# Optimization experiments

Measured on AMD Instinct MI355X. Metric: run time of the kernel, lower is better.

The kernel has to match this reference:

```python
import jax, jax.numpy as jnp
import numpy as np


def dwconv3x3(x, w, b):
    # depthwise 3x3, stride 1, padding 1 (SAME); x: [B,C,H,W], w: [C,1,3,3], b: [C]
    y = jax.lax.conv_general_dilated(
        x, w, window_strides=(1, 1), padding='SAME',
        dimension_numbers=('NCHW', 'OIHW', 'NCHW'),
        feature_group_count=x.shape[1])
    return y + b[None, :, None, None]


def setup_inputs() -> dict:
    B, C, K, H, W = 16, 512, 128, 64, 64
    key = jax.random.key(0)
    ks = jax.random.split(key, 8)
    return {
        'x_q': jax.random.normal(ks[0], (B, C, H, W), jnp.float32),
        'x_kv': jax.random.normal(ks[1], (B, K, H, W), jnp.float32),
        'wq': jax.random.normal(ks[2], (C, 1, 3, 3), jnp.float32) * 0.1,
        'bq': jax.random.normal(ks[3], (C,), jnp.float32) * 0.1,
        'wk': jax.random.normal(ks[4], (K, 1, 3, 3), jnp.float32) * 0.1,
        'bk': jax.random.normal(ks[5], (K,), jnp.float32) * 0.1,
        'wv': jax.random.normal(ks[6], (K, 1, 3, 3), jnp.float32) * 0.1,
        'bv': jax.random.normal(ks[7], (K,), jnp.float32) * 0.1,
    }


def reference(x_q, x_kv, wq, bq, wk, bk, wv, bv):
    q = dwconv3x3(x_q, wq, bq)          # [B,C,H,W]
    k = dwconv3x3(x_kv, wk, bk)         # [B,K,H,W]
    v = dwconv3x3(x_kv, wv, bv)         # [B,K,H,W]
    B, C, H, W = q.shape
    Kp = k.shape[1]
    qf = q.reshape(B, C, H * W)         # [B,C,N]
    kf = k.reshape(B, Kp, H * W)        # [B,K,N]
    vf = v.reshape(B, Kp, H * W)        # [B,K,N]
    # attn_weights: [B,C,K], scaled by sqrt(num_prompt)
    aw = jnp.einsum('bcn,bkn->bck', qf, kf) / (Kp ** 0.5)
    aw = jax.nn.softmax(aw, axis=-1)
    n_keep = int(0.1 * C)               # static
    aw_t = jnp.swapaxes(aw, 1, 2)       # [B,K,C]
    _, idx = jax.lax.top_k(aw_t, n_keep)  # idx: [B,K,n_keep]
    bi = jnp.arange(B)[:, None, None]
    ki = jnp.arange(Kp)[None, :, None]
    mask_t = jnp.zeros_like(aw_t).at[bi, ki, idx].set(1.0)
    aw = aw * jnp.swapaxes(mask_t, 1, 2)  # [B,C,K]
    attn_out = jnp.einsum('bck,bkn->bcn', aw, vf).reshape(B, C, H, W)
    return (x_q + attn_out, aw)
```

## Files before the change

### kernel.cpp

```cpp
#include <hip/hip_runtime.h>

#define B_ 16
#define C_ 512
#define K_ 128
#define N_ 4096
#define NKEEP 51
#define NSPLIT 16

__global__ __launch_bounds__(256) void conv_kv_kernel(const float* __restrict__ xkv,
                               const float* __restrict__ wk, const float* __restrict__ bk,
                               const float* __restrict__ wv, const float* __restrict__ bv,
                               float* __restrict__ kb, float* __restrict__ vb) {
    int idx = blockIdx.x * 256 + threadIdx.x;
    int xs = (idx & 3) << 4;
    int y  = (idx >> 2) & 63;
    int k  = (idx >> 8) & 127;
    int b  = idx >> 15;
    const float* wkp = wk + k * 9;
    const float* wvp = wv + k * 9;
    const float* xp  = xkv + (size_t)(b * K_ + k) * N_;
    float ak[16], av[16];
    float bk0 = bk[k], bv0 = bv[k];
#pragma unroll
    for (int i = 0; i < 16; ++i) { ak[i] = bk0; av[i] = bv0; }
#pragma unroll
    for (int dy = 0; dy < 3; ++dy) {
        int yy = y + dy - 1;
        if (yy < 0 || yy > 63) continue;
        const float* row = xp + yy * 64 + xs;
        const float4* r4 = (const float4*)row;
        float4 m0 = r4[0], m1 = r4[1], m2 = r4[2], m3 = r4[3];
        float xrow[18];
        xrow[0] = (xs == 0) ? 0.f : row[-1];
        xrow[1] = m0.x;  xrow[2] = m0.y;  xrow[3] = m0.z;  xrow[4] = m0.w;
        xrow[5] = m1.x;  xrow[6] = m1.y;  xrow[7] = m1.z;  xrow[8] = m1.w;
        xrow[9] = m2.x;  xrow[10] = m2.y; xrow[11] = m2.z; xrow[12] = m2.w;
        xrow[13] = m3.x; xrow[14] = m3.y; xrow[15] = m3.z; xrow[16] = m3.w;
        xrow[17] = (xs == 48) ? 0.f : row[16];
        float ka = wkp[dy * 3], kb_ = wkp[dy * 3 + 1], kc_ = wkp[dy * 3 + 2];
        float va = wvp[dy * 3], vb_ = wvp[dy * 3 + 1], vc_ = wvp[dy * 3 + 2];
#pragma unroll
        for (int i = 0; i < 16; ++i) {
            ak[i] += xrow[i] * ka + xrow[i + 1] * kb_ + xrow[i + 2] * kc_;
            av[i] += xrow[i] * va + xrow[i + 1] * vb_ + xrow[i + 2] * vc_;
        }
    }
    size_t o = (size_t)(b * K_ + k) * N_ + y * 64 + xs;
    float4* kd = (float4*)(kb + o);
    float4* vd = (float4*)(vb + o);
#pragma unroll
    for (int m = 0; m < 4; ++m) {
        kd[m] = make_float4(ak[4*m], ak[4*m+1], ak[4*m+2], ak[4*m+3]);
        vd[m] = make_float4(av[4*m], av[4*m+1], av[4*m+2], av[4*m+3]);
    }
}

__global__ __launch_bounds__(256) void qk5_kernel(const float* __restrict__ xq,
                                                  const float* __restrict__ wq,
                                                  const float* __restrict__ bq,
                                                  const float* __restrict__ kb,
                                                  float* __restrict__ part) {
    __shared__ float qs[64][64];
    __shared__ float ks[64][128];
    int blk = blockIdx.x;
    int ct  = blk & 7;
    int ns  = (blk >> 3) & 15;
    int b   = blk >> 7;
    int c0  = ct * 64;
    int r0  = ns * 4;
    int tid = threadIdx.x;

    int c_l = tid >> 2;
    int xs  = (tid & 3) << 4;
    int k_l = tid >> 1;
    int nh  = (tid & 1) << 5;
    int cg4 = (tid & 15) * 4;
    int kg8 = (tid >> 4) * 8;

    const float* wp = wq + (size_t)(c0 + c_l) * 9;
    float w00=wp[0],w01=wp[1],w02=wp[2],w10=wp[3],w11=wp[4],w12=wp[5],w20=wp[6],w21=wp[7],w22=wp[8];
    float bias = bq[c0 + c_l];
    const float* xqp = xq + ((size_t)(b * C_) + c0 + c_l) * N_;
    const float* kbp = kb + ((size_t)(b * K_) + k_l) * N_;

    float acc[4][8];
#pragma unroll
    for (int i = 0; i < 4; ++i)
#pragma unroll
        for (int j = 0; j < 8; ++j) acc[i][j] = 0.f;

    for (int rr = 0; rr < 4; ++rr) {
        int r = r0 + rr;
        __syncthreads();
        {
            const float4* src = (const float4*)(kbp + r * 64 + nh);
#pragma unroll
            for (int m = 0; m < 8; ++m) {
                float4 v = src[m];
                int nn = nh + m * 4;
                ks[nn][k_l] = v.x; ks[nn + 1][k_l] = v.y;
                ks[nn + 2][k_l] = v.z; ks[nn + 3][k_l] = v.w;
            }
        }
        {
            float a16[16];
#pragma unroll
            for (int i = 0; i < 16; ++i) a16[i] = bias;
#pragma unroll
            for (int dy = 0; dy < 3; ++dy) {
                int yy = r + dy - 1;
                if (yy < 0 || yy > 63) continue;
                const float* row = xqp + yy * 64;
                float wa = (dy == 0) ? w00 : (dy == 1) ? w10 : w20;
                float wb = (dy == 0) ? w01 : (dy == 1) ? w11 : w21;
                float wc = (dy == 0) ? w02 : (dy == 1) ? w12 : w22;
                float p = (xs == 0) ? 0.f : row[xs - 1];
                float c = row[xs];
#pragma unroll
                for (int i = 0; i < 16; ++i) {
                    int x = xs + i;
                    float n = (x == 63) ? 0.f : row[x + 1];
                    a16[i] += p * wa + c * wb + n * wc;
                    p = c; c = n;
                }
            }
#pragma unroll
            for (int i = 0; i < 16; ++i) qs[xs + i][c_l] = a16[i];
        }
        __syncthreads();
#pragma unroll 4
        for (int nn = 0; nn < 64; ++nn) {
            float4 q4  = *(const float4*)&qs[nn][cg4];
            float4 k4a = *(const float4*)&ks[nn][kg8];
            float4 k4b = *(const float4*)&ks[nn][kg8 + 4];
            float qa[4] = {q4.x, q4.y, q4.z, q4.w};
            float kk[8] = {k4a.x, k4a.y, k4a.z, k4a.w, k4b.x, k4b.y, k4b.z, k4b.w};
#pragma unroll
            for (int i = 0; i < 4; ++i)
#pragma unroll
                for (int j = 0; j < 8; ++j) acc[i][j] += qa[i] * kk[j];
        }
    }
    float* dst = part + (((size_t)ns * B_ + b) * C_ + c0 + cg4) * K_ + kg8;
#pragma unroll
    for (int i = 0; i < 4; ++i) {
        *(float4*)(dst + (size_t)i * K_)     = make_float4(acc[i][0], acc[i][1], acc[i][2], acc[i][3]);
        *(float4*)(dst + (size_t)i * K_ + 4) = make_float4(acc[i][4], acc[i][5], acc[i][6], acc[i][7]);
    }
}

__global__ void softmax_kernel(const float* __restrict__ part, float* __restrict__ aw) {
    int tid  = threadIdx.x;
    int wave = tid >> 6;
    int lane = tid & 63;
    int row  = blockIdx.x * 4 + wave;
    float v0 = 0.f, v1 = 0.f;
#pragma unroll
    for (int ns = 0; ns < NSPLIT; ++ns) {
        const float* p = part + ((size_t)ns * B_ * C_ + row) * K_;
        v0 += p[lane];
        v1 += p[lane + 64];
    }
    const float scale = 0.08838834764831845f;
    v0 *= scale; v1 *= scale;
    float m = fmaxf(v0, v1);
#pragma unroll
    for (int s = 32; s >= 1; s >>= 1) m = fmaxf(m, __shfl_xor(m, s, 64));
    float e0 = __expf(v0 - m), e1 = __expf(v1 - m);
    float s = e0 + e1;
#pragma unroll
    for (int t = 32; t >= 1; t >>= 1) s += __shfl_xor(s, t, 64);
    float inv = 1.0f / s;
    float* q = aw + (size_t)row * K_;
    q[lane] = e0 * inv;
    q[lane + 64] = e1 * inv;
}

__global__ void topk_mask_kernel(float* __restrict__ aw) {
    int tid  = threadIdx.x;
    int wave = tid >> 6, lane = tid & 63;
    int col  = blockIdx.x * 4 + wave;
    int b = col >> 7, k = col & 127;
    float* base = aw + (size_t)(b * C_) * K_ + k;
    unsigned u[8];
#pragma unroll
    for (int j = 0; j < 8; ++j)
        u[j] = __float_as_uint(base[(size_t)(j * 64 + lane) * K_]);
    unsigned T = 0;
#pragma unroll
    for (int bit = 31; bit >= 0; --bit) {
        unsigned cand = T | (1u << bit);
        int cnt = 0;
#pragma unroll
        for (int j = 0; j < 8; ++j) cnt += (u[j] >= cand) ? 1 : 0;
#pragma unroll
        for (int s = 32; s >= 1; s >>= 1) cnt += __shfl_xor(cnt, s, 64);
        if (cnt >= NKEEP) T = cand;
    }
#pragma unroll
    for (int j = 0; j < 8; ++j)
        if (u[j] < T) base[(size_t)(j * 64 + lane) * K_] = 0.0f;
}

__global__ __launch_bounds__(256) void av_kernel(const float* __restrict__ aw,
                                                 const float* __restrict__ vb,
                                                 const float* __restrict__ xq,
                                                 float* __restrict__ out) {
    __shared__ float vs[16][260];
    __shared__ float aws[16][36];
    int blk  = blockIdx.x;
    int b    = blk >> 8;
    int rest = blk & 255;
    int c0 = (rest >> 4) * 32;
    int n0 = (rest & 15) * 256;
    int tid = threadIdx.x;
    int cg = tid >> 5;
    int ng = tid & 31;
    int k_l = tid >> 4;
    int nn0 = (tid & 15) * 16;

    float acc[4][8];
#pragma unroll
    for (int i = 0; i < 4; ++i)
#pragma unroll
        for (int j = 0; j < 8; ++j) acc[i][j] = 0.f;

    for (int kc = 0; kc < K_; kc += 16) {
        __syncthreads();
        {
            const float4* src = (const float4*)(vb + (size_t)(b * K_ + kc + k_l) * N_ + n0 + nn0);
            float4* dst = (float4*)&vs[k_l][nn0];
#pragma unroll
            for (int m = 0; m < 4; ++m) dst[m] = src[m];
        }
        {
            int i0 = tid * 2;
#pragma unroll
            for (int t2 = 0; t2 < 2; ++t2) {
                int i = i0 + t2;
                int cc = i >> 4;
                int kk = i & 15;
                aws[kk][cc] = aw[(size_t)(b * C_ + c0 + cc) * K_ + kc + kk];
            }
        }
        __syncthreads();
#pragma unroll
        for (int kk = 0; kk < 16; ++kk) {
            float4 a4  = *(const float4*)&aws[kk][cg * 4];
            float4 v4a = *(const float4*)&vs[kk][ng * 8];
            float4 v4b = *(const float4*)&vs[kk][ng * 8 + 4];
            float aa[4] = {a4.x, a4.y, a4.z, a4.w};
            float av[8] = {v4a.x, v4a.y, v4a.z, v4a.w, v4b.x, v4b.y, v4b.z, v4b.w};
#pragma unroll
            for (int i = 0; i < 4; ++i)
#pragma unroll
                for (int j = 0; j < 8; ++j) acc[i][j] += aa[i] * av[j];
        }
    }
#pragma unroll
    for (int i = 0; i < 4; ++i) {
        int c = c0 + cg * 4 + i;
        size_t base = (size_t)(b * C_ + c) * N_ + n0 + ng * 8;
        const float4* xp4 = (const float4*)(xq + base);
        float4* op4 = (float4*)(out + base);
        float4 x0 = xp4[0], x1 = xp4[1];
        float4 o0, o1;
        o0.x = x0.x + acc[i][0]; o0.y = x0.y + acc[i][1];
        o0.z = x0.z + acc[i][2]; o0.w = x0.w + acc[i][3];
        o1.x = x1.x + acc[i][4]; o1.y = x1.y + acc[i][5];
        o1.z = x1.z + acc[i][6]; o1.w = x1.w + acc[i][7];
        op4[0] = o0; op4[1] = o1;
    }
}

extern "C" void kernel_launch(void* const* d_in, const int* in_sizes, int n_in,
                              void* d_out, int out_size, void* d_ws, size_t ws_size,
                              hipStream_t stream) {
    const float* xq  = (const float*)d_in[0];
    const float* xkv = (const float*)d_in[1];
    const float* wq  = (const float*)d_in[2];
    const float* bq  = (const float*)d_in[3];
    const float* wk  = (const float*)d_in[4];
    const float* bk  = (const float*)d_in[5];
    const float* wv  = (const float*)d_in[6];
    const float* bv  = (const float*)d_in[7];

    float* out0 = (float*)d_out;
    float* aw   = out0 + (size_t)B_ * C_ * N_;

    float* kb = (float*)d_ws;
    float* vb = kb + (size_t)B_ * K_ * N_;
    float* part = out0;

    conv_kv_kernel<<<(B_ * K_ * 64 * 4) / 256, 256, 0, stream>>>(xkv, wk, bk, wv, bv, kb, vb);
    qk5_kernel<<<B_ * 128, 256, 0, stream>>>(xq, wq, bq, kb, part);
    softmax_kernel<<<(B_ * C_) / 4, 256, 0, stream>>>(part, aw);
    topk_mask_kernel<<<(B_ * K_) / 4, 256, 0, stream>>>(aw);
    av_kernel<<<B_ * 256, 256, 0, stream>>>(aw, vb, xq, out0);
}
```

Measured before the change: 531.7 us.

## Halve QK shared tiles, reorder block mapping, and drop LDS staging in AV

The QK kernel now processes each image row in two 32-column halves, which halves its shared-memory tiles (qs/ks) so more blocks can be resident per CU. Its block index is remapped so consecutive blocks cover different row splits of the same channel tile. The AV kernel drops its shared-memory staging and syncthreads and reads aw and V straight from global memory into registers, relying on cache for reuse. The trade-offs are twice as many barriers in QK and more redundant global/L2 traffic in AV, since V rows are re-read by each channel-group warp.

```diff
diff --git a/kernel.cpp b/kernel.cpp
--- a/kernel.cpp
+++ b/kernel.cpp
@@ -55,25 +55,25 @@
     }
 }
 
-__global__ __launch_bounds__(256) void qk5_kernel(const float* __restrict__ xq,
+__global__ __launch_bounds__(256) void qk6_kernel(const float* __restrict__ xq,
                                                   const float* __restrict__ wq,
                                                   const float* __restrict__ bq,
                                                   const float* __restrict__ kb,
                                                   float* __restrict__ part) {
-    __shared__ float qs[64][64];
-    __shared__ float ks[64][128];
+    __shared__ float qs[32][64];
+    __shared__ float ks[32][128];
     int blk = blockIdx.x;
-    int ct  = blk & 7;
-    int ns  = (blk >> 3) & 15;
+    int ns  = blk & 15;
+    int ct  = (blk >> 4) & 7;
     int b   = blk >> 7;
     int c0  = ct * 64;
     int r0  = ns * 4;
     int tid = threadIdx.x;
 
     int c_l = tid >> 2;
-    int xs  = (tid & 3) << 4;
+    int xb8 = (tid & 3) << 3;
     int k_l = tid >> 1;
-    int nh  = (tid & 1) << 5;
+    int nh  = (tid & 1) << 4;
     int cg4 = (tid & 15) * 4;
     int kg8 = (tid >> 4) * 8;
 
@@ -91,54 +91,58 @@
 
     for (int rr = 0; rr < 4; ++rr) {
         int r = r0 + rr;
-        __syncthreads();
-        {
-            const float4* src = (const float4*)(kbp + r * 64 + nh);
-#pragma unroll
-            for (int m = 0; m < 8; ++m) {
-                float4 v = src[m];
-                int nn = nh + m * 4;
-                ks[nn][k_l] = v.x; ks[nn + 1][k_l] = v.y;
-                ks[nn + 2][k_l] = v.z; ks[nn + 3][k_l] = v.w;
-            }
-        }
-        {
-            float a16[16];
-#pragma unroll
-            for (int i = 0; i < 16; ++i) a16[i] = bias;
-#pragma unroll
-            for (int dy = 0; dy < 3; ++dy) {
-                int yy = r + dy - 1;
-                if (yy < 0 || yy > 63) continue;
-                const float* row = xqp + yy * 64;
-                float wa = (dy == 0) ? w00 : (dy == 1) ? w10 : w20;
-                float wb = (dy == 0) ? w01 : (dy == 1) ? w11 : w21;
-                float wc = (dy == 0) ? w02 : (dy == 1) ? w12 : w22;
-                float p = (xs == 0) ? 0.f : row[xs - 1];
-                float c = row[xs];
-#pragma unroll
-                for (int i = 0; i < 16; ++i) {
-                    int x = xs + i;
-                    float n = (x == 63) ? 0.f : row[x + 1];
-                    a16[i] += p * wa + c * wb + n * wc;
-                    p = c; c = n;
+#pragma unroll
+        for (int h = 0; h < 2; ++h) {
+            __syncthreads();
+            {
+                const float4* src = (const float4*)(kbp + r * 64 + h * 32 + nh);
+#pragma unroll
+                for (int m = 0; m < 4; ++m) {
+                    float4 v = src[m];
+                    int nn = nh + m * 4;
+                    ks[nn][k_l] = v.x; ks[nn + 1][k_l] = v.y;
+                    ks[nn + 2][k_l] = v.z; ks[nn + 3][k_l] = v.w;
                 }
             }
-#pragma unroll
-            for (int i = 0; i < 16; ++i) qs[xs + i][c_l] = a16[i];
-        }
-        __syncthreads();
+            {
+                int x0 = xb8 + h * 32;
+                float a8[8];
+#pragma unroll
+                for (int i = 0; i < 8; ++i) a8[i] = bias;
+#pragma unroll
+                for (int dy = 0; dy < 3; ++dy) {
+                    int yy = r + dy - 1;
+                    if (yy < 0 || yy > 63) continue;
+                    const float* row = xqp + yy * 64;
+                    float wa = (dy == 0) ? w00 : (dy == 1) ? w10 : w20;
+                    float wb = (dy == 0) ? w01 : (dy == 1) ? w11 : w21;
+                    float wc = (dy == 0) ? w02 : (dy == 1) ? w12 : w22;
+                    float p = (x0 == 0) ? 0.f : row[x0 - 1];
+                    float c = row[x0];
+#pragma unroll
+                    for (int i = 0; i < 8; ++i) {
+                        int x = x0 + i;
+                        float nx = (x == 63) ? 0.f : row[x + 1];
+                        a8[i] += p * wa + c * wb + nx * wc;
+                        p = c; c = nx;
+                    }
+                }
+#pragma unroll
+                for (int i = 0; i < 8; ++i) qs[xb8 + i][c_l] = a8[i];
+            }
+            __syncthreads();
 #pragma unroll 4
-        for (int nn = 0; nn < 64; ++nn) {
-            float4 q4  = *(const float4*)&qs[nn][cg4];
-            float4 k4a = *(const float4*)&ks[nn][kg8];
-            float4 k4b = *(const float4*)&ks[nn][kg8 + 4];
-            float qa[4] = {q4.x, q4.y, q4.z, q4.w};
-            float kk[8] = {k4a.x, k4a.y, k4a.z, k4a.w, k4b.x, k4b.y, k4b.z, k4b.w};
-#pragma unroll
-            for (int i = 0; i < 4; ++i)
-#pragma unroll
-                for (int j = 0; j < 8; ++j) acc[i][j] += qa[i] * kk[j];
+            for (int nn = 0; nn < 32; ++nn) {
+                float4 q4  = *(const float4*)&qs[nn][cg4];
+                float4 k4a = *(const float4*)&ks[nn][kg8];
+                float4 k4b = *(const float4*)&ks[nn][kg8 + 4];
+                float qa[4] = {q4.x, q4.y, q4.z, q4.w};
+                float kk[8] = {k4a.x, k4a.y, k4a.z, k4a.w, k4b.x, k4b.y, k4b.z, k4b.w};
+#pragma unroll
+                for (int i = 0; i < 4; ++i)
+#pragma unroll
+                    for (int j = 0; j < 8; ++j) acc[i][j] += qa[i] * kk[j];
+            }
         }
     }
     float* dst = part + (((size_t)ns * B_ + b) * C_ + c0 + cg4) * K_ + kg8;
@@ -202,12 +206,10 @@
         if (u[j] < T) base[(size_t)(j * 64 + lane) * K_] = 0.0f;
 }
 
-__global__ __launch_bounds__(256) void av_kernel(const float* __restrict__ aw,
-                                                 const float* __restrict__ vb,
-                                                 const float* __restrict__ xq,
-                                                 float* __restrict__ out) {
-    __shared__ float vs[16][260];
-    __shared__ float aws[16][36];
+__global__ __launch_bounds__(256) void av2_kernel(const float* __restrict__ aw,
+                                                  const float* __restrict__ vb,
+                                                  const float* __restrict__ xq,
+                                                  float* __restrict__ out) {
     int blk  = blockIdx.x;
     int b    = blk >> 8;
     int rest = blk & 255;
@@ -216,8 +218,9 @@
     int tid = threadIdx.x;
     int cg = tid >> 5;
     int ng = tid & 31;
-    int k_l = tid >> 4;
-    int nn0 = (tid & 15) * 16;
+
+    const float* awp = aw + (size_t)(b * C_ + c0 + cg * 4) * K_;
+    const float* vbp = vb + (size_t)(b * K_) * N_ + n0 + ng * 8;
 
     float acc[4][8];
 #pragma unroll
@@ -225,36 +228,26 @@
 #pragma unroll
         for (int j = 0; j < 8; ++j) acc[i][j] = 0.f;
 
-    for (int kc = 0; kc < K_; kc += 16) {
-        __syncthreads();
-        {
-            const float4* src = (const float4*)(vb + (size_t)(b * K_ + kc + k_l) * N_ + n0 + nn0);
-            float4* dst = (float4*)&vs[k_l][nn0];
-#pragma unroll
-            for (int m = 0; m < 4; ++m) dst[m] = src[m];
-        }
-        {
-            int i0 = tid * 2;
-#pragma unroll
-            for (int t2 = 0; t2 < 2; ++t2) {
-                int i = i0 + t2;
-                int cc = i >> 4;
-                int kk = i & 15;
-                aws[kk][cc] = aw[(size_t)(b * C_ + c0 + cc) * K_ + kc + kk];
-            }
-        }
-        __syncthreads();
-#pragma unroll
-        for (int kk = 0; kk < 16; ++kk) {
-            float4 a4  = *(const float4*)&aws[kk][cg * 4];
-            float4 v4a = *(const float4*)&vs[kk][ng * 8];
-            float4 v4b = *(const float4*)&vs[kk][ng * 8 + 4];
-            float aa[4] = {a4.x, a4.y, a4.z, a4.w};
-            float av[8] = {v4a.x, v4a.y, v4a.z, v4a.w, v4b.x, v4b.y, v4b.z, v4b.w};
+    for (int kc = 0; kc < K_; kc += 4) {
+        float4 a0 = *(const float4*)(awp + 0 * K_ + kc);
+        float4 a1 = *(const float4*)(awp + 1 * K_ + kc);
+        float4 a2 = *(const float4*)(awp + 2 * K_ + kc);
+        float4 a3 = *(const float4*)(awp + 3 * K_ + kc);
+#pragma unroll
+        for (int j = 0; j < 4; ++j) {
+            const float* vrow = vbp + (size_t)(kc + j) * N_;
+            float4 v0 = *(const float4*)(vrow);
+            float4 v1 = *(const float4*)(vrow + 4);
+            float aa[4];
+            aa[0] = (j == 0) ? a0.x : (j == 1) ? a0.y : (j == 2) ? a0.z : a0.w;
+            aa[1] = (j == 0) ? a1.x : (j == 1) ? a1.y : (j == 2) ? a1.z : a1.w;
+            aa[2] = (j == 0) ? a2.x : (j == 1) ? a2.y : (j == 2) ? a2.z : a2.w;
+            aa[3] = (j == 0) ? a3.x : (j == 1) ? a3.y : (j == 2) ? a3.z : a3.w;
+            float av[8] = {v0.x, v0.y, v0.z, v0.w, v1.x, v1.y, v1.z, v1.w};
 #pragma unroll
             for (int i = 0; i < 4; ++i)
 #pragma unroll
-                for (int j = 0; j < 8; ++j) acc[i][j] += aa[i] * av[j];
+                for (int jj = 0; jj < 8; ++jj) acc[i][jj] += aa[i] * av[jj];
         }
     }
 #pragma unroll
@@ -293,8 +286,8 @@
     float* part = out0;
 
     conv_kv_kernel<<<(B_ * K_ * 64 * 4) / 256, 256, 0, stream>>>(xkv, wk, bk, wv, bv, kb, vb);
-    qk5_kernel<<<B_ * 128, 256, 0, stream>>>(xq, wq, bq, kb, part);
+    qk6_kernel<<<B_ * 128, 256, 0, stream>>>(xq, wq, bq, kb, part);
     softmax_kernel<<<(B_ * C_) / 4, 256, 0, stream>>>(part, aw);
     topk_mask_kernel<<<(B_ * K_) / 4, 256, 0, stream>>>(aw);
-    av_kernel<<<B_ * 256, 256, 0, stream>>>(aw, vb, xq, out0);
-}
+    av2_kernel<<<B_ * 256, 256, 0, stream>>>(aw, vb, xq, out0);
+}
```

After: 646.1 us. 1.22x slower.
